# Performance work log

Measured on AMD Instinct MI355X. Metric: run time of the kernel, lower is better.

The kernel has to match this reference:

```python
import jax, jax.numpy as jnp
import numpy as np

N_QUBITS = 8
N_LAYERS = 4
BATCH = 8192


def _ry_mat(theta):
    # RY(theta) = [[cos(t/2), -sin(t/2)], [sin(t/2), cos(t/2)]]; theta scalar or (B,)
    c = jnp.cos(theta * 0.5)
    s = jnp.sin(theta * 0.5)
    return jnp.stack([jnp.stack([c, -s], -1), jnp.stack([s, c], -1)], -2).astype(jnp.complex64)


def _apply_1q(state, U, wire):
    # U: (2,2) gate shared across batch; state: (B, 2,...,2) with axis wire+1 = target wire
    s = jnp.moveaxis(state, wire + 1, -1)
    s = jnp.einsum('ij,...j->...i', U, s)
    return jnp.moveaxis(s, -1, wire + 1)


def _apply_1q_batched(state, U, wire):
    # U: (B,2,2) per-sample gate (data-dependent RY angles)
    s = jnp.moveaxis(state, wire + 1, -1)
    s = jnp.einsum('bij,b...j->b...i', U, s)
    return jnp.moveaxis(s, -1, wire + 1)


def _apply_rz(state, theta, wire):
    # RZ is diagonal: multiply amplitudes by exp(-i t/2) / exp(+i t/2)
    phases = jnp.stack([jnp.exp(-0.5j * theta), jnp.exp(0.5j * theta)]).astype(jnp.complex64)
    s = jnp.moveaxis(state, wire + 1, -1)
    s = s * phases
    return jnp.moveaxis(s, -1, wire + 1)


def _cnot(state, c, t):
    # flip target amplitudes on the control=1 subspace
    s = jnp.moveaxis(state, (c + 1, t + 1), (-2, -1))
    s = jnp.stack([s[..., 0, :], s[..., 1, ::-1]], axis=-2)
    return jnp.moveaxis(s, (-2, -1), (c + 1, t + 1))


def _forward(x, weights):
    B = x.shape[0]
    state = jnp.zeros((B,) + (2,) * N_QUBITS, jnp.complex64)
    state = state.at[(slice(None),) + (0,) * N_QUBITS].set(1.0)  # |0...0>
    # data-encoding RY layer (angles depend on inputs -> per-sample gates)
    for i in range(N_QUBITS):
        state = _apply_1q_batched(state, _ry_mat(x[:, i] + weights[0, i, 0]), i)
    # entangling + rotation layers
    for layer in range(N_LAYERS):
        for i in range(N_QUBITS - 1):
            state = _cnot(state, i, i + 1)
        state = _cnot(state, N_QUBITS - 1, 0)
        for i in range(N_QUBITS):
            state = _apply_rz(state, weights[layer, i, 1], i)
            state = _apply_1q(state, _ry_mat(weights[layer, i, 0]), i)
    # <Z_i> = p(wire_i = 0) - p(wire_i = 1)
    p = state.real ** 2 + state.imag ** 2
    all_axes = tuple(range(1, N_QUBITS + 1))
    outs = []
    for i in range(N_QUBITS):
        m = p.sum(axis=tuple(a for a in all_axes if a != i + 1))  # (B, 2)
        outs.append(m[:, 0] - m[:, 1])
    return jnp.stack(outs, axis=1)  # (B, N_QUBITS)


def setup_inputs() -> dict:
    key = jax.random.key(0)
    k1, k2 = jax.random.split(key)
    x = jax.random.normal(k1, (BATCH, N_QUBITS), jnp.float32)
    weights = jax.random.normal(k2, (N_LAYERS, N_QUBITS, 2), jnp.float32)
    return {"x": x, "weights": weights}


def reference(x, weights):
    return _forward(x, weights)
```

## Files before the change

### kernel.cpp

```cpp
#include <hip/hip_runtime.h>

#define BATCH 8192

typedef __attribute__((ext_vector_type(8))) short bf16x8;
typedef __attribute__((ext_vector_type(4))) float f32x4;

__device__ __forceinline__ unsigned short f2bf(float f) {
    unsigned int u = __float_as_uint(f);
    u += 0x7fffu + ((u >> 16) & 1u);
    return (unsigned short)(u >> 16);
}
__device__ __forceinline__ float rdl(float v, int lane) {
    return __int_as_float(__builtin_amdgcn_readlane(__float_as_int(v), lane));
}

__global__ __launch_bounds__(64) void ukern(const float* __restrict__ w,
                                            unsigned short* __restrict__ Ub)
{
    const int l = threadIdx.x;
    const int c = blockIdx.x;

    float v0, v1, v2, v3;
    {
        const int t  = l & 31;
        const int li = t >> 3;
        const int wi = t & 7;
        float th = w[(li * 8 + wi) * 2 + 0];
        float ph = w[(li * 8 + wi) * 2 + 1];
        float cth = __cosf(0.5f * th), sth = __sinf(0.5f * th);
        if (wi < 6) {
            float cph = __cosf(0.5f * ph), sph = __sinf(0.5f * ph);
            v0 = cth * cph;  v1 = cth * sph;  v2 = sth * cph;  v3 = sth * sph;
        } else {
            v0 = cth;  v1 = sth;  v2 = __cosf(ph);  v3 = __sinf(ph);
        }
    }

    float re[4], im[4];
    const bool ls = (l == (c >> 2));
    #pragma unroll
    for (int k = 0; k < 4; ++k) {
        re[k] = (ls && ((c & 3) == k)) ? 1.0f : 0.0f;
        im[k] = 0.0f;
    }
    const int  src = (l ^ (l >> 1)) & 63;
    const bool c5  = (l & 1);

    #pragma unroll
    for (int layer = 0; layer < 4; ++layer) {
        const int lb = layer * 8;
        float tr[4], ti[4];
        #pragma unroll
        for (int k = 0; k < 4; ++k) {
            tr[k] = __shfl(re[k], src, 64);
            ti[k] = __shfl(im[k], src, 64);
        }
        re[0] = c5 ? tr[2] : tr[0];  im[0] = c5 ? ti[2] : ti[0];
        re[1] = c5 ? tr[3] : tr[1];  im[1] = c5 ? ti[3] : ti[1];
        re[2] = c5 ? tr[1] : tr[3];  im[2] = c5 ? ti[1] : ti[3];
        re[3] = c5 ? tr[0] : tr[2];  im[3] = c5 ? ti[0] : ti[2];
        re[1] = __shfl_xor(re[1], 32, 64); im[1] = __shfl_xor(im[1], 32, 64);
        re[3] = __shfl_xor(re[3], 32, 64); im[3] = __shfl_xor(im[3], 32, 64);

        #pragma unroll
        for (int i = 0; i < 6; ++i) {
            float Ar = rdl(v0, lb + i);
            float SZ = rdl(v3, lb + i);
            float sgn = (l & (32 >> i)) ? 1.0f : -1.0f;
            float Ai = sgn * rdl(v1, lb + i);
            float Br = sgn * rdl(v2, lb + i);
            const int m = 32 >> i;
            #pragma unroll
            for (int k = 0; k < 4; ++k) {
                float br = __shfl_xor(re[k], m, 64);
                float bi = __shfl_xor(im[k], m, 64);
                float ar = re[k], ai = im[k];
                re[k] = Ar*ar - Ai*ai + Br*br + SZ*bi;
                im[k] = Ar*ai + Ai*ar + Br*bi - SZ*br;
            }
        }
        #pragma unroll
        for (int i = 0; i < 2; ++i) {
            float cy = rdl(v0, lb + 6 + i);
            float sy = rdl(v1, lb + 6 + i);
            float cf = rdl(v2, lb + 6 + i);
            float sf = rdl(v3, lb + 6 + i);
            const int mk = 2 >> i;
            #pragma unroll
            for (int k = 0; k < 4; ++k) {
                if (!(k & mk)) continue;
                float r = re[k], q = im[k];
                re[k] = r * cf - q * sf;
                im[k] = q * cf + r * sf;
            }
            #pragma unroll
            for (int k = 0; k < 4; ++k) {
                if (k & mk) continue;
                int k1 = k | mk;
                float ar = re[k], ai = im[k], br = re[k1], bi = im[k1];
                re[k]  = cy * ar - sy * br;
                im[k]  = cy * ai - sy * bi;
                re[k1] = sy * ar + cy * br;
                im[k1] = sy * ai + cy * bi;
            }
        }
    }
    #pragma unroll
    for (int k = 0; k < 4; ++k) {
        int i = l * 4 + k;
        Ub[i * 256 + c]         = f2bf(re[k]);
        Ub[(256 + i) * 256 + c] = f2bf(im[k]);
    }
}

__global__ __launch_bounds__(512, 2) void qmain(const float* __restrict__ x,
                                                const float* __restrict__ w,
                                                const unsigned short* __restrict__ Ub,
                                                float* __restrict__ out)
{
    __shared__ float trg[32][17];
    __shared__ unsigned short psi[32 * 264];
    __shared__ float Ps[8][289];
    const int tid  = threadIdx.x;
    const int wid  = tid >> 6;
    const int lane = tid & 63;
    const int bid  = blockIdx.x;
    const int s0   = bid * 32;

    const int mrow = lane & 15;
    const int kgrp = lane >> 4;
    const int sblk = wid * 4 + (lane >> 4);

    const int wi = lane & 7;
    float xv = 0.f;
    if ((lane & 15) < 8)
        xv = x[(s0 + sblk) * 8 + wi];

    bf16x8 apf[4][8];
    #pragma unroll
    for (int ks = 0; ks < 8; ++ks) {
        const int k0 = ks * 32 + kgrp * 8;
        #pragma unroll
        for (int mt = 0; mt < 4; ++mt) {
            const int row = (mt < 2) ? (wid * 32 + mt * 16 + mrow)
                                     : (256 + wid * 32 + (mt - 2) * 16 + mrow);
            apf[mt][ks] = *(const bf16x8*)(Ub + row * 256 + k0);
        }
    }

    if ((lane & 15) < 8) {
        float a = 0.5f * (xv + w[2 * wi]);
        trg[sblk][wi]     = __cosf(a);
        trg[sblk][8 + wi] = __sinf(a);
    }

    {
        const int s  = sblk;
        const int j1 = lane & 15;
        float c0 = trg[s][0], c1 = trg[s][1], c2 = trg[s][2], c3 = trg[s][3];
        float s0w = trg[s][8], s1w = trg[s][9], s2w = trg[s][10], s3w = trg[s][11];
        float A1 = ((j1 & 8) ? s0w : c0) * ((j1 & 4) ? s1w : c1)
                 * ((j1 & 2) ? s2w : c2) * ((j1 & 1) ? s3w : c3);
        float c4 = trg[s][4], c5 = trg[s][5], c6 = trg[s][6], c7 = trg[s][7];
        float s4 = trg[s][12], s5 = trg[s][13], s6 = trg[s][14], s7 = trg[s][15];
        float q45[4] = {A1 * c4 * c5, A1 * c4 * s5, A1 * s4 * c5, A1 * s4 * s5};
        float p67[4] = {c6 * c7, c6 * s7, s6 * c7, s6 * s7};
        unsigned int wbuf[8];
        #pragma unroll
        for (int p = 0; p < 8; ++p) {
            int ja = 2 * p, jb = 2 * p + 1;
            float va = q45[ja >> 2] * p67[ja & 3];
            float vb = q45[jb >> 2] * p67[jb & 3];
            wbuf[p] = (unsigned int)f2bf(va) | ((unsigned int)f2bf(vb) << 16);
        }
        uint4* dst = (uint4*)((char*)psi + s * 528 + j1 * 32);
        dst[0] = make_uint4(wbuf[0], wbuf[1], wbuf[2], wbuf[3]);
        dst[1] = make_uint4(wbuf[4], wbuf[5], wbuf[6], wbuf[7]);
    }
    __syncthreads();

    f32x4 acc[4][2];
    #pragma unroll
    for (int a = 0; a < 4; ++a)
        #pragma unroll
        for (int b = 0; b < 2; ++b)
            acc[a][b] = (f32x4){0.f, 0.f, 0.f, 0.f};

    #pragma unroll
    for (int ks = 0; ks < 8; ++ks) {
        const int k0 = ks * 32 + kgrp * 8;
        bf16x8 bfr0 = *(const bf16x8*)(psi + mrow * 264 + k0);
        bf16x8 bfr1 = *(const bf16x8*)(psi + (16 + mrow) * 264 + k0);
        #pragma unroll
        for (int mt = 0; mt < 4; ++mt) {
            acc[mt][0] = __builtin_amdgcn_mfma_f32_16x16x32_bf16(apf[mt][ks], bfr0, acc[mt][0], 0, 0, 0);
            acc[mt][1] = __builtin_amdgcn_mfma_f32_16x16x32_bf16(apf[mt][ks], bfr1, acc[mt][1], 0, 0, 0);
        }
    }

    #pragma unroll
    for (int nt = 0; nt < 2; ++nt) {
        float am[2], r2m[2], r1m[2];
        #pragma unroll
        for (int mtl = 0; mtl < 2; ++mtl) {
            float p0 = acc[mtl][nt][0]*acc[mtl][nt][0] + acc[mtl+2][nt][0]*acc[mtl+2][nt][0];
            float p1 = acc[mtl][nt][1]*acc[mtl][nt][1] + acc[mtl+2][nt][1]*acc[mtl+2][nt][1];
            float p2 = acc[mtl][nt][2]*acc[mtl][nt][2] + acc[mtl+2][nt][2]*acc[mtl+2][nt][2];
            float p3 = acc[mtl][nt][3]*acc[mtl][nt][3] + acc[mtl+2][nt][3]*acc[mtl+2][nt][3];
            float t0 = p0 + p1, t1 = p2 + p3;
            am[mtl]  = t0 + t1;
            r2m[mtl] = t0 - t1;
            r1m[mtl] = (p0 - p1) + (p2 - p3);
        }
        float ps = am[0] + am[1];
        float m3 = am[0] - am[1];
        float m6 = r2m[0] + r2m[1];
        float m7 = r1m[0] + r1m[1];
        float m0 = (wid & 4)  ? -ps : ps;
        float m1 = (wid & 2)  ? -ps : ps;
        float m2 = (wid & 1)  ? -ps : ps;
        float m4 = (kgrp & 2) ? -ps : ps;
        float m5 = (kgrp & 1) ? -ps : ps;
        m0 += __shfl_xor(m0, 16, 64);  m0 += __shfl_xor(m0, 32, 64);
        m1 += __shfl_xor(m1, 16, 64);  m1 += __shfl_xor(m1, 32, 64);
        m2 += __shfl_xor(m2, 16, 64);  m2 += __shfl_xor(m2, 32, 64);
        m3 += __shfl_xor(m3, 16, 64);  m3 += __shfl_xor(m3, 32, 64);
        m4 += __shfl_xor(m4, 16, 64);  m4 += __shfl_xor(m4, 32, 64);
        m5 += __shfl_xor(m5, 16, 64);  m5 += __shfl_xor(m5, 32, 64);
        m6 += __shfl_xor(m6, 16, 64);  m6 += __shfl_xor(m6, 32, 64);
        m7 += __shfl_xor(m7, 16, 64);  m7 += __shfl_xor(m7, 32, 64);
        if (kgrp == 0) {
            const int snt = nt * 16 + mrow;
            float* pp = &Ps[wid][snt * 9];
            pp[0]=m0; pp[1]=m1; pp[2]=m2; pp[3]=m3; pp[4]=m4; pp[5]=m5; pp[6]=m6; pp[7]=m7;
        }
    }
    __syncthreads();
    if (tid < 64) {
        const int s    = tid & 31;
        const int half = tid >> 5;
        float r0 = 0.f, r1 = 0.f, r2 = 0.f, r3 = 0.f;
        #pragma unroll
        for (int uu = 0; uu < 8; ++uu) {
            const float* pp = &Ps[uu][s * 9 + half * 4];
            r0 += pp[0]; r1 += pp[1]; r2 += pp[2]; r3 += pp[3];
        }
        float4* o = (float4*)(out + (s0 + s) * 8 + half * 4);
        *o = make_float4(r0, r1, r2, r3);
    }
}

extern "C" void kernel_launch(void* const* d_in, const int* in_sizes, int n_in,
                              void* d_out, int out_size, void* d_ws, size_t ws_size,
                              hipStream_t stream)
{
    const float* x = (const float*)d_in[0];
    const float* w = (const float*)d_in[1];
    unsigned short* Ub = (unsigned short*)d_ws;
    ukern<<<256, 64, 0, stream>>>(w, Ub);
    qmain<<<256, 512, 0, stream>>>(x, w, Ub, (float*)d_out);
}
```

Measured before the change: 23.02 us.

## Process 64 samples per block and stream U fragments from memory per k-step

Each block now handles 64 samples instead of 32, so the grid halves to 128 blocks and each loaded U fragment feeds four MFMA N-tiles instead of two. The U matrix is no longer preloaded into a 32-register array up front; fragments are loaded from global memory inside the k-loop. The aim is to halve total U traffic and reduce register pressure. The cost is only 128 blocks on a GPU with more CUs, plus load latency exposed inside the MFMA loop.

```diff
diff --git a/kernel.cpp b/kernel.cpp
--- a/kernel.cpp
+++ b/kernel.cpp
@@ -113,50 +113,37 @@
     }
 }
 
-__global__ __launch_bounds__(512, 2) void qmain(const float* __restrict__ x,
-                                                const float* __restrict__ w,
-                                                const unsigned short* __restrict__ Ub,
-                                                float* __restrict__ out)
+__global__ __launch_bounds__(512) void qmain(const float* __restrict__ x,
+                                             const float* __restrict__ w,
+                                             const unsigned short* __restrict__ Ub,
+                                             float* __restrict__ out)
 {
-    __shared__ float trg[32][17];
-    __shared__ unsigned short psi[32 * 264];
-    __shared__ float Ps[8][289];
+    __shared__ float trg[64][17];
+    __shared__ unsigned short psi[64 * 264];
+    __shared__ float Ps[8][580];
     const int tid  = threadIdx.x;
     const int wid  = tid >> 6;
     const int lane = tid & 63;
     const int bid  = blockIdx.x;
-    const int s0   = bid * 32;
+    const int s0   = bid * 64;
 
     const int mrow = lane & 15;
     const int kgrp = lane >> 4;
-    const int sblk = wid * 4 + (lane >> 4);
-
-    const int wi = lane & 7;
-    float xv = 0.f;
-    if ((lane & 15) < 8)
-        xv = x[(s0 + sblk) * 8 + wi];
-
-    bf16x8 apf[4][8];
-    #pragma unroll
-    for (int ks = 0; ks < 8; ++ks) {
-        const int k0 = ks * 32 + kgrp * 8;
-        #pragma unroll
-        for (int mt = 0; mt < 4; ++mt) {
-            const int row = (mt < 2) ? (wid * 32 + mt * 16 + mrow)
-                                     : (256 + wid * 32 + (mt - 2) * 16 + mrow);
-            apf[mt][ks] = *(const bf16x8*)(Ub + row * 256 + k0);
-        }
-    }
-
-    if ((lane & 15) < 8) {
-        float a = 0.5f * (xv + w[2 * wi]);
-        trg[sblk][wi]     = __cosf(a);
-        trg[sblk][8 + wi] = __sinf(a);
-    }
+    const int sp   = (tid >> 4) * 2;
+    const int lam  = lane & 15;
 
     {
-        const int s  = sblk;
-        const int j1 = lane & 15;
+        const int sA = sp + (lam >> 3);
+        const int wi = lam & 7;
+        float a = 0.5f * (x[(s0 + sA) * 8 + wi] + w[2 * wi]);
+        trg[sA][wi]     = __cosf(a);
+        trg[sA][8 + wi] = __sinf(a);
+    }
+
+    #pragma unroll
+    for (int j = 0; j < 2; ++j) {
+        const int s  = sp + j;
+        const int j1 = lam;
         float c0 = trg[s][0], c1 = trg[s][1], c2 = trg[s][2], c3 = trg[s][3];
         float s0w = trg[s][8], s1w = trg[s][9], s2w = trg[s][10], s3w = trg[s][11];
         float A1 = ((j1 & 8) ? s0w : c0) * ((j1 & 4) ? s1w : c1)
@@ -179,27 +166,33 @@
     }
     __syncthreads();
 
-    f32x4 acc[4][2];
+    f32x4 acc[4][4];
     #pragma unroll
     for (int a = 0; a < 4; ++a)
         #pragma unroll
-        for (int b = 0; b < 2; ++b)
+        for (int b = 0; b < 4; ++b)
             acc[a][b] = (f32x4){0.f, 0.f, 0.f, 0.f};
 
     #pragma unroll
     for (int ks = 0; ks < 8; ++ks) {
         const int k0 = ks * 32 + kgrp * 8;
-        bf16x8 bfr0 = *(const bf16x8*)(psi + mrow * 264 + k0);
-        bf16x8 bfr1 = *(const bf16x8*)(psi + (16 + mrow) * 264 + k0);
+        bf16x8 bfr[4];
+        #pragma unroll
+        for (int nt = 0; nt < 4; ++nt)
+            bfr[nt] = *(const bf16x8*)(psi + (nt * 16 + mrow) * 264 + k0);
         #pragma unroll
         for (int mt = 0; mt < 4; ++mt) {
-            acc[mt][0] = __builtin_amdgcn_mfma_f32_16x16x32_bf16(apf[mt][ks], bfr0, acc[mt][0], 0, 0, 0);
-            acc[mt][1] = __builtin_amdgcn_mfma_f32_16x16x32_bf16(apf[mt][ks], bfr1, acc[mt][1], 0, 0, 0);
-        }
-    }
-
-    #pragma unroll
-    for (int nt = 0; nt < 2; ++nt) {
+            const int row = (mt < 2) ? (wid * 32 + mt * 16 + mrow)
+                                     : (256 + wid * 32 + (mt - 2) * 16 + mrow);
+            bf16x8 afr = *(const bf16x8*)(Ub + row * 256 + k0);
+            #pragma unroll
+            for (int nt = 0; nt < 4; ++nt)
+                acc[mt][nt] = __builtin_amdgcn_mfma_f32_16x16x32_bf16(afr, bfr[nt], acc[mt][nt], 0, 0, 0);
+        }
+    }
+
+    #pragma unroll
+    for (int nt = 0; nt < 4; ++nt) {
         float am[2], r2m[2], r1m[2];
         #pragma unroll
         for (int mtl = 0; mtl < 2; ++mtl) {
@@ -236,9 +229,9 @@
         }
     }
     __syncthreads();
-    if (tid < 64) {
-        const int s    = tid & 31;
-        const int half = tid >> 5;
+    if (tid < 128) {
+        const int s    = tid & 63;
+        const int half = tid >> 6;
         float r0 = 0.f, r1 = 0.f, r2 = 0.f, r3 = 0.f;
         #pragma unroll
         for (int uu = 0; uu < 8; ++uu) {
@@ -258,5 +251,5 @@
     const float* w = (const float*)d_in[1];
     unsigned short* Ub = (unsigned short*)d_ws;
     ukern<<<256, 64, 0, stream>>>(w, Ub);
-    qmain<<<256, 512, 0, stream>>>(x, w, Ub, (float*)d_out);
-}
+    qmain<<<128, 512, 0, stream>>>(x, w, Ub, (float*)d_out);
+}
```

Measured after the change: 24.09 us. 1.05x slower.
